# Optimization experiments

Measured on AMD Instinct MI355X. Metric: run time of the kernel, lower is better.

The kernel has to match this reference:

```python
import jax, jax.numpy as jnp
import numpy as np

N = 4096      # nodes
IN = 512      # in_dim
HID = 64      # hid_dim
OUT = 8       # out_dim (classes)
H = 2         # num_heads / meta-paths
SEM = 32      # semantic attention hidden size
P_EDGE = 0.005  # edge probability -> avg degree ~20


def setup_inputs() -> dict:
    key = jax.random.key(0)
    ks = jax.random.split(key, 12)
    h = jax.random.normal(ks[0], (N, IN), jnp.float32)
    # sparse binary adjacency per head, with self-loops (densified as in adj.to_dense())
    adj = (jax.random.uniform(ks[1], (H, N, N)) < P_EDGE).astype(jnp.float32)
    adj = jnp.clip(adj + jnp.eye(N, dtype=jnp.float32)[None], 0.0, 1.0)
    sc = lambda k, s: (jax.random.normal(k, s, jnp.float32) * 0.05)
    W1 = sc(ks[2], (H, IN, HID))
    b1 = jnp.zeros((H, HID), jnp.float32)
    Wq = sc(ks[3], (H, HID, HID)); bq = jnp.zeros((H, HID), jnp.float32)
    Wk = sc(ks[4], (H, HID, HID)); bk = jnp.zeros((H, HID), jnp.float32)
    Wv = sc(ks[5], (H, HID, HID)); bv = jnp.zeros((H, HID), jnp.float32)
    sem_W1 = sc(ks[6], (HID, SEM)); sem_b1 = jnp.zeros((SEM,), jnp.float32)
    sem_W2 = sc(ks[7], (SEM, 1))
    pred_W = sc(ks[8], (HID, OUT)); pred_b = jnp.zeros((OUT,), jnp.float32)
    return dict(h=h, adj=adj, W1=W1, b1=b1, Wq=Wq, bq=bq, Wk=Wk, bk=bk,
                Wv=Wv, bv=bv, sem_W1=sem_W1, sem_b1=sem_b1, sem_W2=sem_W2,
                pred_W=pred_W, pred_b=pred_b)


def reference(h, adj, W1, b1, Wq, bq, Wk, bk, Wv, bv,
              sem_W1, sem_b1, sem_W2, pred_W, pred_b):
    def embed(adj_i, W1_i, b1_i, Wq_i, bq_i, Wk_i, bk_i, Wv_i, bv_i):
        # GraphConvolution (Kipf): adj @ (h @ W) + b, then ReLU
        x = jax.nn.relu(adj_i @ (h @ W1_i) + b1_i)            # [N, HID]
        Q = x @ Wq_i + bq_i
        K = x @ Wk_i + bk_i
        V = x @ Wv_i + bv_i
        # dense-masked attention: adj.to_dense() * (Q K^T), softmax over rows
        A_tilde = adj_i * (Q @ K.T)                            # [N, N]
        att = jax.nn.softmax(A_tilde, axis=1)
        # gcn_norm: symmetric D^{-1/2} A D^{-1/2}, degree = row sums
        d = att.sum(axis=1)
        dinv = jnp.where(d > 0, jax.lax.rsqrt(d), 0.0)
        att_n = dinv[:, None] * att * dinv[None, :]
        return jax.nn.relu(att_n @ V)                          # [N, HID]

    z = jax.vmap(embed)(adj, W1, b1, Wq, bq, Wk, bk, Wv, bv)   # [H, N, HID]
    z = jnp.transpose(z, (1, 0, 2))                            # [N, H, HID]
    # SemanticAttention: project -> mean over nodes -> softmax over dim=1
    w = jnp.tanh(z @ sem_W1 + sem_b1) @ sem_W2                 # [N, H, 1]
    w = w.mean(axis=0)                                         # [H, 1]
    beta = jax.nn.softmax(w, axis=1)  # faithful to torch.softmax(w, dim=1)
    p2 = (beta[None] * z).sum(axis=1)                          # [N, HID]
    return jax.nn.softmax(p2 @ pred_W + pred_b, axis=1)        # [N, OUT]
```

## Files before the change

kernel.cpp:

```cpp
#include <hip/hip_runtime.h>
#include <hip/hip_bf16.h>

#define NN   4096
#define IND  512
#define HIDD 64
#define OUTD 8
#define NH   2
#define CAP  128

using bf16 = __hip_bfloat16;

__device__ __forceinline__ float b2f(bf16 v) { return __bfloat162float(v); }

__device__ __forceinline__ bool sniff_bf(const unsigned* __restrict__ adjw) {
    return (adjw[0] & 0xFFFFu) == 0x3F80u;
}
__device__ __forceinline__ float ldf(const void* p, int i, bool isbf) {
    return isbf ? b2f(((const bf16*)p)[i]) : ((const float*)p)[i];
}
__device__ __forceinline__ void load8f(const void* p, size_t off, bool isbf, float* o) {
    if (isbf) {
        uint4 d = *reinterpret_cast<const uint4*>((const bf16*)p + off);
        unsigned u[4] = {d.x, d.y, d.z, d.w};
#pragma unroll
        for (int w = 0; w < 4; ++w) {
            o[2 * w]     = __uint_as_float(u[w] << 16);
            o[2 * w + 1] = __uint_as_float(u[w] & 0xFFFF0000u);
        }
    } else {
        const float* q = (const float*)p + off;
        float4 a = *reinterpret_cast<const float4*>(q);
        float4 b = *reinterpret_cast<const float4*>(q + 4);
        o[0] = a.x; o[1] = a.y; o[2] = a.z; o[3] = a.w;
        o[4] = b.x; o[5] = b.y; o[6] = b.z; o[7] = b.w;
    }
}
__device__ __forceinline__ void load8_f32(const float* q, float* o) {
    float4 a = *reinterpret_cast<const float4*>(q);
    float4 b = *reinterpret_cast<const float4*>(q + 4);
    o[0] = a.x; o[1] = a.y; o[2] = a.z; o[3] = a.w;
    o[4] = b.x; o[5] = b.y; o[6] = b.z; o[7] = b.w;
}

__global__ void __launch_bounds__(256) k1_csr_hw(const void* __restrict__ h,
                                                 const void* __restrict__ W1,
                                                 const void* __restrict__ adjv,
                                                 int* __restrict__ deg,
                                                 int* __restrict__ cols,
                                                 float* __restrict__ hW,
                                                 float* __restrict__ vsum) {
    __shared__ __align__(16) float As[64][36];
    __shared__ __align__(16) float Bs[64][68];
    __shared__ int s_cnt;
    __shared__ int s_lc[CAP];
    const bool isbf = sniff_bf((const unsigned*)adjv);
    const int bx = blockIdx.x;
    const int tid = threadIdx.x;
    if (bx == 0 && tid < NH * HIDD) vsum[tid] = 0.f;

    if (bx < 256) {
        int head = bx >> 7;
        int i0 = (bx & 127) * 32;
        size_t wOff = (size_t)head * IND * HIDD;
        int r0 = (tid >> 4) * 2;
        int c0 = (tid & 15) * 4;
        float acc[2][4] = {};
        for (int kc = 0; kc < IND; kc += 64) {
            {
                int row = tid >> 3;
                int kp  = (tid & 7) * 8;
                float t8[8];
                load8f(h, (size_t)(i0 + row) * IND + kc + kp, isbf, t8);
#pragma unroll
                for (int j = 0; j < 8; ++j) As[kp + j][row] = t8[j];
            }
            {
                int kb = tid >> 2;
                int cp = (tid & 3) * 16;
                float t8[8];
                load8f(W1, wOff + (size_t)(kc + kb) * HIDD + cp, isbf, t8);
#pragma unroll
                for (int j = 0; j < 8; ++j) Bs[kb][cp + j] = t8[j];
                load8f(W1, wOff + (size_t)(kc + kb) * HIDD + cp + 8, isbf, t8);
#pragma unroll
                for (int j = 0; j < 8; ++j) Bs[kb][cp + 8 + j] = t8[j];
            }
            __syncthreads();
#pragma unroll 8
            for (int k = 0; k < 64; ++k) {
                float2 a2 = *reinterpret_cast<const float2*>(&As[k][r0]);
                float4 b4 = *reinterpret_cast<const float4*>(&Bs[k][c0]);
                float bb[4] = {b4.x, b4.y, b4.z, b4.w};
#pragma unroll
                for (int ib = 0; ib < 4; ++ib) {
                    acc[0][ib] = fmaf(a2.x, bb[ib], acc[0][ib]);
                    acc[1][ib] = fmaf(a2.y, bb[ib], acc[1][ib]);
                }
            }
            __syncthreads();
        }
        float* Ch = hW + (size_t)head * NN * HIDD;
#pragma unroll
        for (int ia = 0; ia < 2; ++ia)
            *reinterpret_cast<float4*>(Ch + (size_t)(i0 + r0 + ia) * HIDD + c0) =
                make_float4(acc[ia][0], acc[ia][1], acc[ia][2], acc[ia][3]);
        return;
    }
    int row = bx - 256;
    if (tid == 0) s_cnt = 0;
    __syncthreads();
    if (isbf) {
        const uint4* a4 = reinterpret_cast<const uint4*>((const bf16*)adjv + (size_t)row * NN);
#pragma unroll
        for (int it = 0; it < 2; ++it) {
            int v = tid + it * 256;
            uint4 d = a4[v];
            unsigned u[4] = {d.x, d.y, d.z, d.w};
            int base = v * 8;
#pragma unroll
            for (int w = 0; w < 4; ++w) {
                if (u[w] & 0xFFFFu) { int p = atomicAdd(&s_cnt, 1); if (p < CAP) s_lc[p] = base + 2 * w; }
                if (u[w] >> 16)     { int p = atomicAdd(&s_cnt, 1); if (p < CAP) s_lc[p] = base + 2 * w + 1; }
            }
        }
    } else {
        const uint4* a4 = reinterpret_cast<const uint4*>((const float*)adjv + (size_t)row * NN);
#pragma unroll
        for (int it = 0; it < 4; ++it) {
            int v = tid + it * 256;
            uint4 d = a4[v];
            unsigned u[4] = {d.x, d.y, d.z, d.w};
            int base = v * 4;
#pragma unroll
            for (int w = 0; w < 4; ++w) {
                if (u[w]) { int p = atomicAdd(&s_cnt, 1); if (p < CAP) s_lc[p] = base + w; }
            }
        }
    }
    __syncthreads();
    int c = s_cnt; if (c > CAP) c = CAP;
    if (tid == 0) deg[row] = c;
    int* oc = cols + (size_t)row * CAP;
    for (int k = tid; k < c; k += 256) oc[k] = s_lc[k];
}

__global__ void k_aggx(const float* __restrict__ hW, const void* __restrict__ b1,
                       const void* __restrict__ adjv,
                       const int* __restrict__ deg, const int* __restrict__ cols,
                       float* __restrict__ x) {
    bool isbf = sniff_bf((const unsigned*)adjv);
    int h = blockIdx.y;
    int i = blockIdx.x * 4 + threadIdx.y;
    int t = threadIdx.x;
    const float* hWh = hW + (size_t)h * NN * HIDD;
    int r = h * NN + i;
    int d = deg[r];
    const int* cl = cols + (size_t)r * CAP;
    float acc = ldf(b1, h * HIDD + t, isbf);
    int e = 0;
    for (; e + 4 <= d; e += 4) {
        int c0 = cl[e], c1 = cl[e + 1], c2 = cl[e + 2], c3 = cl[e + 3];
        float v0 = hWh[(size_t)c0 * HIDD + t];
        float v1 = hWh[(size_t)c1 * HIDD + t];
        float v2 = hWh[(size_t)c2 * HIDD + t];
        float v3 = hWh[(size_t)c3 * HIDD + t];
        acc += (v0 + v1) + (v2 + v3);
    }
    for (; e < d; ++e) acc += hWh[(size_t)cl[e] * HIDD + t];
    x[(size_t)r * HIDD + t] = fmaxf(acc, 0.f);
}

__global__ void __launch_bounds__(256) k_qkv(const float* __restrict__ x,
                                             const void* Wq, const void* bq,
                                             const void* Wk, const void* bk,
                                             const void* Wv, const void* bv,
                                             const void* __restrict__ adjv,
                                             float* Q, float* K, float* V,
                                             float* __restrict__ vsum) {
    __shared__ __align__(16) float xs[64][36];
    __shared__ __align__(16) float Ws[64][68];
    __shared__ float vred[HIDD];
    bool isbf = sniff_bf((const unsigned*)adjv);
    int tid = threadIdx.x;
    int z = blockIdx.x >> 8;
    int rem = blockIdx.x & 255;
    int head = rem >> 7;
    int i0 = (rem & 127) * 32;
    const void* W  = (z == 0) ? Wq : (z == 1) ? Wk : Wv;
    const void* bb = (z == 0) ? bq : (z == 1) ? bk : bv;
    float* C = ((z == 0) ? Q : (z == 1) ? K : V) + (size_t)head * NN * HIDD;
    const float* xh = x + (size_t)head * NN * HIDD;
    {
        int row = tid >> 3;
        int kp  = (tid & 7) * 8;
        float t8[8];
        load8_f32(xh + (size_t)(i0 + row) * HIDD + kp, t8);
#pragma unroll
        for (int j = 0; j < 8; ++j) xs[kp + j][row] = t8[j];
    }
    {
        int kb = tid >> 2;
        int cp = (tid & 3) * 16;
        size_t base = (size_t)head * HIDD * HIDD + (size_t)kb * HIDD + cp;
        float t8[8];
        load8f(W, base, isbf, t8);
#pragma unroll
        for (int j = 0; j < 8; ++j) Ws[kb][cp + j] = t8[j];
        load8f(W, base + 8, isbf, t8);
#pragma unroll
        for (int j = 0; j < 8; ++j) Ws[kb][cp + 8 + j] = t8[j];
    }
    if (tid < HIDD) vred[tid] = 0.f;
    __syncthreads();
    int r0 = (tid >> 4) * 2;
    int c0 = (tid & 15) * 4;
    float acc[2][4] = {};
#pragma unroll 8
    for (int k = 0; k < HIDD; ++k) {
        float2 a2 = *reinterpret_cast<const float2*>(&xs[k][r0]);
        float4 b4 = *reinterpret_cast<const float4*>(&Ws[k][c0]);
        float bbv[4] = {b4.x, b4.y, b4.z, b4.w};
#pragma unroll
        for (int ib = 0; ib < 4; ++ib) {
            acc[0][ib] = fmaf(a2.x, bbv[ib], acc[0][ib]);
            acc[1][ib] = fmaf(a2.y, bbv[ib], acc[1][ib]);
        }
    }
    float bz[4];
#pragma unroll
    for (int ib = 0; ib < 4; ++ib) bz[ib] = ldf(bb, head * HIDD + c0 + ib, isbf);
#pragma unroll
    for (int ia = 0; ia < 2; ++ia)
        *reinterpret_cast<float4*>(C + (size_t)(i0 + r0 + ia) * HIDD + c0) =
            make_float4(acc[ia][0] + bz[0], acc[ia][1] + bz[1],
                        acc[ia][2] + bz[2], acc[ia][3] + bz[3]);
    if (z == 2) {
#pragma unroll
        for (int ib = 0; ib < 4; ++ib)
            atomicAdd(&vred[c0 + ib], acc[0][ib] + acc[1][ib] + 2.f * bz[ib]);
        __syncthreads();
        if (tid < HIDD) atomicAdd(&vsum[head * HIDD + tid], vred[tid]);
    }
}

__global__ void __launch_bounds__(256) k_attn(const float* __restrict__ Q,
                                              const float* __restrict__ Km,
                                              const float* __restrict__ V,
                                              const float* __restrict__ vsum,
                                              const int* __restrict__ deg,
                                              const int* __restrict__ cols,
                                              const void* __restrict__ predW,
                                              const void* __restrict__ predb,
                                              const void* __restrict__ adjv,
                                              void* __restrict__ outv) {
    bool isbf = sniff_bf((const unsigned*)adjv);
    int wid = threadIdx.x >> 6;
    int t   = threadIdx.x & 63;
    int i   = blockIdx.x * 4 + wid;
    __shared__ __align__(16) float qs[4][64];
    __shared__ float wgt[4][CAP];
    __shared__ int   cs[4][CAP];
    __shared__ float p2s[4][64];
    float p2 = 0.f;

    for (int h = 0; h < NH; ++h) {
        int r = h * NN + i;
        int d = deg[r];
        const int* cl   = cols + (size_t)r * CAP;
        const float* Qh = Q + (size_t)h * NN * HIDD;
        const float* Kh = Km + (size_t)h * NN * HIDD;
        const float* Vh = V + (size_t)h * NN * HIDD;
        qs[wid][t] = Qh[(size_t)i * HIDD + t];
        for (int e = t; e < d; e += 64) cs[wid][e] = cl[e];

        float s0 = 0.f, s1 = 0.f;
        float lmax = 0.f;
        const float4* q4 = reinterpret_cast<const float4*>(qs[wid]);
        if (t < d) {
            const float4* K4 = reinterpret_cast<const float4*>(Kh + (size_t)cs[wid][t] * HIDD);
            float s = 0.f;
#pragma unroll 4
            for (int k = 0; k < 16; ++k) {
                float4 kv = K4[k]; float4 qv = q4[k];
                s += qv.x * kv.x + qv.y * kv.y + qv.z * kv.z + qv.w * kv.w;
            }
            s0 = s; lmax = fmaxf(lmax, s);
        }
        if (t + 64 < d) {
            const float4* K4 = reinterpret_cast<const float4*>(Kh + (size_t)cs[wid][t + 64] * HIDD);
            float s = 0.f;
#pragma unroll 4
            for (int k = 0; k < 16; ++k) {
                float4 kv = K4[k]; float4 qv = q4[k];
                s += qv.x * kv.x + qv.y * kv.y + qv.z * kv.z + qv.w * kv.w;
            }
            s1 = s; lmax = fmaxf(lmax, s);
        }
#pragma unroll
        for (int off = 32; off; off >>= 1) lmax = fmaxf(lmax, __shfl_xor(lmax, off));
        float m  = lmax;
        float eb = __expf(-m);
        float lsum = 0.f;
        if (t < d)      { float w = __expf(s0 - m); lsum += w; wgt[wid][t] = w - eb; }
        if (t + 64 < d) { float w = __expf(s1 - m); lsum += w; wgt[wid][t + 64] = w - eb; }
#pragma unroll
        for (int off = 32; off; off >>= 1) lsum += __shfl_xor(lsum, off);
        float Z = lsum + (float)(NN - d) * eb;
        float c = 1.f / Z;

        float acc = eb * vsum[h * HIDD + t];
        int e = 0;
        for (; e + 4 <= d; e += 4) {
            float w0 = wgt[wid][e], w1 = wgt[wid][e + 1];
            float w2 = wgt[wid][e + 2], w3 = wgt[wid][e + 3];
            int c0 = cs[wid][e], c1 = cs[wid][e + 1];
            int c2 = cs[wid][e + 2], c3 = cs[wid][e + 3];
            float v0 = Vh[(size_t)c0 * HIDD + t];
            float v1 = Vh[(size_t)c1 * HIDD + t];
            float v2 = Vh[(size_t)c2 * HIDD + t];
            float v3 = Vh[(size_t)c3 * HIDD + t];
            acc += w0 * v0 + w1 * v1 + w2 * v2 + w3 * v3;
        }
        for (; e < d; ++e) acc += wgt[wid][e] * Vh[(size_t)cs[wid][e] * HIDD + t];
        p2 += fmaxf(acc * c, 0.f);
    }

    p2s[wid][t] = p2;
    if (t < OUTD) {
        float a = ldf(predb, t, isbf);
#pragma unroll 8
        for (int k = 0; k < HIDD; ++k) a += p2s[wid][k] * ldf(predW, k * OUTD + t, isbf);
        float mx = a;
#pragma unroll
        for (int off = 4; off; off >>= 1) mx = fmaxf(mx, __shfl_xor(mx, off));
        float e = __expf(a - mx);
        float s = e;
#pragma unroll
        for (int off = 4; off; off >>= 1) s += __shfl_xor(s, off);
        float v = e / s;
        if (isbf) ((bf16*)outv)[(size_t)i * OUTD + t] = __float2bfloat16(v);
        else      ((float*)outv)[(size_t)i * OUTD + t] = v;
    }
}

extern "C" void kernel_launch(void* const* d_in, const int* in_sizes, int n_in,
                              void* d_out, int out_size, void* d_ws, size_t ws_size,
                              hipStream_t stream) {
    const void* adj = d_in[1];

    char* w = (char*)d_ws;
    int*   deg  = (int*)w;                        w += (size_t)NH * NN * 4;
    int*   cols = (int*)w;                        w += (size_t)NH * NN * CAP * 4;
    float* hW   = (float*)w;                      w += (size_t)NH * NN * HIDD * 4;
    float* x    = (float*)w;                      w += (size_t)NH * NN * HIDD * 4;
    float* Q    = (float*)w;                      w += (size_t)NH * NN * HIDD * 4;
    float* K    = (float*)w;                      w += (size_t)NH * NN * HIDD * 4;
    float* V    = (float*)w;                      w += (size_t)NH * NN * HIDD * 4;
    float* vsum = (float*)w;                      w += (size_t)NH * HIDD * 4;

    k1_csr_hw<<<256 + NH * NN, 256, 0, stream>>>(d_in[0], d_in[2], adj, deg, cols, hW, vsum);
    k_aggx   <<<dim3(NN / 4, NH), dim3(64, 4), 0, stream>>>(hW, d_in[3], adj, deg, cols, x);
    k_qkv    <<<768, 256, 0, stream>>>(x, d_in[4], d_in[5], d_in[6], d_in[7],
                                       d_in[8], d_in[9], adj, Q, K, V, vsum);
    k_attn   <<<NN / 4, 256, 0, stream>>>(Q, K, V, vsum, deg, cols, d_in[13], d_in[14],
                                          adj, d_out);
}
```

Measured before the change: 256.2 us.

## Fuse aggregation, QKV and attention kernels into one persistent kernel with grid barriers

Merges the three post-CSR kernels (neighbour aggregation, QKV projection, sparse attention with prediction) into a single 1024-block kernel that separates the phases with software grid barriers built on global atomics. Shared memory for the phases is overlaid through a union. The aim is to remove two kernel launch gaps and their tail effects. The cost is spin-wait barriers that assume all 1024 blocks are co-resident (launch_bounds 256,4), plus a bounded spin timeout that could break correctness if residency is not met.

```diff
diff --git a/kernel.cpp b/kernel.cpp
--- a/kernel.cpp
+++ b/kernel.cpp
@@ -7,6 +7,7 @@
 #define OUTD 8
 #define NH   2
 #define CAP  128
+#define FBLK 1024
 
 using bf16 = __hip_bfloat16;
 
@@ -48,7 +49,8 @@
                                                  int* __restrict__ deg,
                                                  int* __restrict__ cols,
                                                  float* __restrict__ hW,
-                                                 float* __restrict__ vsum) {
+                                                 float* __restrict__ vsum,
+                                                 int* __restrict__ bar) {
     __shared__ __align__(16) float As[64][36];
     __shared__ __align__(16) float Bs[64][68];
     __shared__ int s_cnt;
@@ -56,7 +58,10 @@
     const bool isbf = sniff_bf((const unsigned*)adjv);
     const int bx = blockIdx.x;
     const int tid = threadIdx.x;
-    if (bx == 0 && tid < NH * HIDD) vsum[tid] = 0.f;
+    if (bx == 0) {
+        if (tid < NH * HIDD) vsum[tid] = 0.f;
+        if (tid < 8) bar[tid] = 0;
+    }
 
     if (bx < 256) {
         int head = bx >> 7;
@@ -144,202 +149,210 @@
     for (int k = tid; k < c; k += 256) oc[k] = s_lc[k];
 }
 
-__global__ void k_aggx(const float* __restrict__ hW, const void* __restrict__ b1,
-                       const void* __restrict__ adjv,
-                       const int* __restrict__ deg, const int* __restrict__ cols,
-                       float* __restrict__ x) {
-    bool isbf = sniff_bf((const unsigned*)adjv);
-    int h = blockIdx.y;
-    int i = blockIdx.x * 4 + threadIdx.y;
-    int t = threadIdx.x;
-    const float* hWh = hW + (size_t)h * NN * HIDD;
-    int r = h * NN + i;
-    int d = deg[r];
-    const int* cl = cols + (size_t)r * CAP;
-    float acc = ldf(b1, h * HIDD + t, isbf);
-    int e = 0;
-    for (; e + 4 <= d; e += 4) {
-        int c0 = cl[e], c1 = cl[e + 1], c2 = cl[e + 2], c3 = cl[e + 3];
-        float v0 = hWh[(size_t)c0 * HIDD + t];
-        float v1 = hWh[(size_t)c1 * HIDD + t];
-        float v2 = hWh[(size_t)c2 * HIDD + t];
-        float v3 = hWh[(size_t)c3 * HIDD + t];
-        acc += (v0 + v1) + (v2 + v3);
-    }
-    for (; e < d; ++e) acc += hWh[(size_t)cl[e] * HIDD + t];
-    x[(size_t)r * HIDD + t] = fmaxf(acc, 0.f);
-}
-
-__global__ void __launch_bounds__(256) k_qkv(const float* __restrict__ x,
-                                             const void* Wq, const void* bq,
-                                             const void* Wk, const void* bk,
-                                             const void* Wv, const void* bv,
-                                             const void* __restrict__ adjv,
-                                             float* Q, float* K, float* V,
-                                             float* __restrict__ vsum) {
-    __shared__ __align__(16) float xs[64][36];
-    __shared__ __align__(16) float Ws[64][68];
-    __shared__ float vred[HIDD];
-    bool isbf = sniff_bf((const unsigned*)adjv);
-    int tid = threadIdx.x;
-    int z = blockIdx.x >> 8;
-    int rem = blockIdx.x & 255;
-    int head = rem >> 7;
-    int i0 = (rem & 127) * 32;
-    const void* W  = (z == 0) ? Wq : (z == 1) ? Wk : Wv;
-    const void* bb = (z == 0) ? bq : (z == 1) ? bk : bv;
-    float* C = ((z == 0) ? Q : (z == 1) ? K : V) + (size_t)head * NN * HIDD;
-    const float* xh = x + (size_t)head * NN * HIDD;
+__device__ __forceinline__ void gridbar(int* bar, int tid) {
+    __builtin_amdgcn_s_waitcnt(0);
+    __syncthreads();
+    if (tid == 0) {
+        __threadfence();
+        __hip_atomic_fetch_add(bar, 1, __ATOMIC_RELEASE, __HIP_MEMORY_SCOPE_AGENT);
+        long spins = 0;
+        while (__hip_atomic_load(bar, __ATOMIC_RELAXED, __HIP_MEMORY_SCOPE_AGENT) < FBLK
+               && ++spins < 4000000L)
+            __builtin_amdgcn_s_sleep(2);
+        __threadfence();
+    }
+    __syncthreads();
+}
+
+struct FArgs {
+    const void *b1, *Wq, *bq, *Wk, *bk, *Wv, *bv, *pW, *pb, *adj;
+    const int *deg, *cols;
+    const float *hW;
+    float *x, *Q, *K, *V, *vsum;
+    int *bar;
+    void *out;
+};
+
+__global__ void __launch_bounds__(256, 4) k_fused(FArgs a) {
+    __shared__ __align__(16) union {
+        struct { float xs[64][36]; float Ws[64][68]; float vred[64]; } q;
+        struct { float qs[4][64]; float wgt[4][CAP]; int cs[4][CAP]; float p2s[4][64]; } t;
+    } su;
+    const bool isbf = sniff_bf((const unsigned*)a.adj);
+    const int bx = blockIdx.x;
+    const int tid = threadIdx.x;
+    const int wv = tid >> 6;
+    const int t  = tid & 63;
+
     {
-        int row = tid >> 3;
-        int kp  = (tid & 7) * 8;
-        float t8[8];
-        load8_f32(xh + (size_t)(i0 + row) * HIDD + kp, t8);
-#pragma unroll
-        for (int j = 0; j < 8; ++j) xs[kp + j][row] = t8[j];
-    }
+        int g = bx * 4 + wv;
+#pragma unroll
+        for (int rr = 0; rr < 2; ++rr) {
+            int r = g * 2 + rr;
+            int h = r >> 12;
+            const float* hWh = a.hW + (size_t)h * NN * HIDD;
+            int d = a.deg[r];
+            const int* cl = a.cols + (size_t)r * CAP;
+            float acc = ldf(a.b1, h * HIDD + t, isbf);
+            int e = 0;
+            for (; e + 4 <= d; e += 4) {
+                int c0 = cl[e], c1 = cl[e + 1], c2 = cl[e + 2], c3 = cl[e + 3];
+                float v0 = hWh[(size_t)c0 * HIDD + t];
+                float v1 = hWh[(size_t)c1 * HIDD + t];
+                float v2 = hWh[(size_t)c2 * HIDD + t];
+                float v3 = hWh[(size_t)c3 * HIDD + t];
+                acc += (v0 + v1) + (v2 + v3);
+            }
+            for (; e < d; ++e) acc += hWh[(size_t)cl[e] * HIDD + t];
+            a.x[(size_t)r * HIDD + t] = fmaxf(acc, 0.f);
+        }
+    }
+    gridbar(&a.bar[0], tid);
+
+    if (bx < 768) {
+        int z = bx >> 8;
+        int rem = bx & 255;
+        int head = rem >> 7;
+        int i0 = (rem & 127) * 32;
+        const void* W  = (z == 0) ? a.Wq : (z == 1) ? a.Wk : a.Wv;
+        const void* bb = (z == 0) ? a.bq : (z == 1) ? a.bk : a.bv;
+        float* C = ((z == 0) ? a.Q : (z == 1) ? a.K : a.V) + (size_t)head * NN * HIDD;
+        const float* xh = a.x + (size_t)head * NN * HIDD;
+        {
+            int row = tid >> 3;
+            int kp  = (tid & 7) * 8;
+            float t8[8];
+            load8_f32(xh + (size_t)(i0 + row) * HIDD + kp, t8);
+#pragma unroll
+            for (int j = 0; j < 8; ++j) su.q.xs[kp + j][row] = t8[j];
+        }
+        {
+            int kb = tid >> 2;
+            int cp = (tid & 3) * 16;
+            size_t base = (size_t)head * HIDD * HIDD + (size_t)kb * HIDD + cp;
+            float t8[8];
+            load8f(W, base, isbf, t8);
+#pragma unroll
+            for (int j = 0; j < 8; ++j) su.q.Ws[kb][cp + j] = t8[j];
+            load8f(W, base + 8, isbf, t8);
+#pragma unroll
+            for (int j = 0; j < 8; ++j) su.q.Ws[kb][cp + 8 + j] = t8[j];
+        }
+        if (tid < HIDD) su.q.vred[tid] = 0.f;
+        __syncthreads();
+        int r0 = (tid >> 4) * 2;
+        int c0 = (tid & 15) * 4;
+        float acc[2][4] = {};
+#pragma unroll 8
+        for (int k = 0; k < HIDD; ++k) {
+            float2 a2 = *reinterpret_cast<const float2*>(&su.q.xs[k][r0]);
+            float4 b4 = *reinterpret_cast<const float4*>(&su.q.Ws[k][c0]);
+            float bbv[4] = {b4.x, b4.y, b4.z, b4.w};
+#pragma unroll
+            for (int ib = 0; ib < 4; ++ib) {
+                acc[0][ib] = fmaf(a2.x, bbv[ib], acc[0][ib]);
+                acc[1][ib] = fmaf(a2.y, bbv[ib], acc[1][ib]);
+            }
+        }
+        float bz[4];
+#pragma unroll
+        for (int ib = 0; ib < 4; ++ib) bz[ib] = ldf(bb, head * HIDD + c0 + ib, isbf);
+#pragma unroll
+        for (int ia = 0; ia < 2; ++ia)
+            *reinterpret_cast<float4*>(C + (size_t)(i0 + r0 + ia) * HIDD + c0) =
+                make_float4(acc[ia][0] + bz[0], acc[ia][1] + bz[1],
+                            acc[ia][2] + bz[2], acc[ia][3] + bz[3]);
+        if (z == 2) {
+#pragma unroll
+            for (int ib = 0; ib < 4; ++ib)
+                atomicAdd(&su.q.vred[c0 + ib], acc[0][ib] + acc[1][ib] + 2.f * bz[ib]);
+            __syncthreads();
+            if (tid < HIDD) atomicAdd(&a.vsum[head * HIDD + tid], su.q.vred[tid]);
+        }
+    }
+    gridbar(&a.bar[1], tid);
+
     {
-        int kb = tid >> 2;
-        int cp = (tid & 3) * 16;
-        size_t base = (size_t)head * HIDD * HIDD + (size_t)kb * HIDD + cp;
-        float t8[8];
-        load8f(W, base, isbf, t8);
-#pragma unroll
-        for (int j = 0; j < 8; ++j) Ws[kb][cp + j] = t8[j];
-        load8f(W, base + 8, isbf, t8);
-#pragma unroll
-        for (int j = 0; j < 8; ++j) Ws[kb][cp + 8 + j] = t8[j];
-    }
-    if (tid < HIDD) vred[tid] = 0.f;
-    __syncthreads();
-    int r0 = (tid >> 4) * 2;
-    int c0 = (tid & 15) * 4;
-    float acc[2][4] = {};
+        int i = bx * 4 + wv;
+        float p2 = 0.f;
+        for (int h = 0; h < NH; ++h) {
+            int r = h * NN + i;
+            int d = a.deg[r];
+            const int* cl   = a.cols + (size_t)r * CAP;
+            const float* Qh = a.Q + (size_t)h * NN * HIDD;
+            const float* Kh = a.K + (size_t)h * NN * HIDD;
+            const float* Vh = a.V + (size_t)h * NN * HIDD;
+            su.t.qs[wv][t] = Qh[(size_t)i * HIDD + t];
+            for (int e = t; e < d; e += 64) su.t.cs[wv][e] = cl[e];
+
+            float s0 = 0.f, s1 = 0.f;
+            float lmax = 0.f;
+            const float4* q4 = reinterpret_cast<const float4*>(su.t.qs[wv]);
+            if (t < d) {
+                const float4* K4 = reinterpret_cast<const float4*>(Kh + (size_t)su.t.cs[wv][t] * HIDD);
+                float s = 0.f;
+#pragma unroll 4
+                for (int k = 0; k < 16; ++k) {
+                    float4 kv = K4[k]; float4 qv = q4[k];
+                    s += qv.x * kv.x + qv.y * kv.y + qv.z * kv.z + qv.w * kv.w;
+                }
+                s0 = s; lmax = fmaxf(lmax, s);
+            }
+            if (t + 64 < d) {
+                const float4* K4 = reinterpret_cast<const float4*>(Kh + (size_t)su.t.cs[wv][t + 64] * HIDD);
+                float s = 0.f;
+#pragma unroll 4
+                for (int k = 0; k < 16; ++k) {
+                    float4 kv = K4[k]; float4 qv = q4[k];
+                    s += qv.x * kv.x + qv.y * kv.y + qv.z * kv.z + qv.w * kv.w;
+                }
+                s1 = s; lmax = fmaxf(lmax, s);
+            }
+#pragma unroll
+            for (int off = 32; off; off >>= 1) lmax = fmaxf(lmax, __shfl_xor(lmax, off));
+            float m  = lmax;
+            float eb = __expf(-m);
+            float lsum = 0.f;
+            if (t < d)      { float w = __expf(s0 - m); lsum += w; su.t.wgt[wv][t] = w - eb; }
+            if (t + 64 < d) { float w = __expf(s1 - m); lsum += w; su.t.wgt[wv][t + 64] = w - eb; }
+#pragma unroll
+            for (int off = 32; off; off >>= 1) lsum += __shfl_xor(lsum, off);
+            float Z = lsum + (float)(NN - d) * eb;
+            float c = 1.f / Z;
+
+            float acc = eb * a.vsum[h * HIDD + t];
+            int e = 0;
+            for (; e + 4 <= d; e += 4) {
+                float w0 = su.t.wgt[wv][e],     w1 = su.t.wgt[wv][e + 1];
+                float w2 = su.t.wgt[wv][e + 2], w3 = su.t.wgt[wv][e + 3];
+                int c0 = su.t.cs[wv][e],     c1 = su.t.cs[wv][e + 1];
+                int c2 = su.t.cs[wv][e + 2], c3 = su.t.cs[wv][e + 3];
+                float v0 = Vh[(size_t)c0 * HIDD + t];
+                float v1 = Vh[(size_t)c1 * HIDD + t];
+                float v2 = Vh[(size_t)c2 * HIDD + t];
+                float v3 = Vh[(size_t)c3 * HIDD + t];
+                acc += w0 * v0 + w1 * v1 + w2 * v2 + w3 * v3;
+            }
+            for (; e < d; ++e) acc += su.t.wgt[wv][e] * Vh[(size_t)su.t.cs[wv][e] * HIDD + t];
+            p2 += fmaxf(acc * c, 0.f);
+        }
+
+        su.t.p2s[wv][t] = p2;
+        if (t < OUTD) {
+            float o = ldf(a.pb, t, isbf);
 #pragma unroll 8
-    for (int k = 0; k < HIDD; ++k) {
-        float2 a2 = *reinterpret_cast<const float2*>(&xs[k][r0]);
-        float4 b4 = *reinterpret_cast<const float4*>(&Ws[k][c0]);
-        float bbv[4] = {b4.x, b4.y, b4.z, b4.w};
-#pragma unroll
-        for (int ib = 0; ib < 4; ++ib) {
-            acc[0][ib] = fmaf(a2.x, bbv[ib], acc[0][ib]);
-            acc[1][ib] = fmaf(a2.y, bbv[ib], acc[1][ib]);
-        }
-    }
-    float bz[4];
-#pragma unroll
-    for (int ib = 0; ib < 4; ++ib) bz[ib] = ldf(bb, head * HIDD + c0 + ib, isbf);
-#pragma unroll
-    for (int ia = 0; ia < 2; ++ia)
-        *reinterpret_cast<float4*>(C + (size_t)(i0 + r0 + ia) * HIDD + c0) =
-            make_float4(acc[ia][0] + bz[0], acc[ia][1] + bz[1],
-                        acc[ia][2] + bz[2], acc[ia][3] + bz[3]);
-    if (z == 2) {
-#pragma unroll
-        for (int ib = 0; ib < 4; ++ib)
-            atomicAdd(&vred[c0 + ib], acc[0][ib] + acc[1][ib] + 2.f * bz[ib]);
-        __syncthreads();
-        if (tid < HIDD) atomicAdd(&vsum[head * HIDD + tid], vred[tid]);
-    }
-}
-
-__global__ void __launch_bounds__(256) k_attn(const float* __restrict__ Q,
-                                              const float* __restrict__ Km,
-                                              const float* __restrict__ V,
-                                              const float* __restrict__ vsum,
-                                              const int* __restrict__ deg,
-                                              const int* __restrict__ cols,
-                                              const void* __restrict__ predW,
-                                              const void* __restrict__ predb,
-                                              const void* __restrict__ adjv,
-                                              void* __restrict__ outv) {
-    bool isbf = sniff_bf((const unsigned*)adjv);
-    int wid = threadIdx.x >> 6;
-    int t   = threadIdx.x & 63;
-    int i   = blockIdx.x * 4 + wid;
-    __shared__ __align__(16) float qs[4][64];
-    __shared__ float wgt[4][CAP];
-    __shared__ int   cs[4][CAP];
-    __shared__ float p2s[4][64];
-    float p2 = 0.f;
-
-    for (int h = 0; h < NH; ++h) {
-        int r = h * NN + i;
-        int d = deg[r];
-        const int* cl   = cols + (size_t)r * CAP;
-        const float* Qh = Q + (size_t)h * NN * HIDD;
-        const float* Kh = Km + (size_t)h * NN * HIDD;
-        const float* Vh = V + (size_t)h * NN * HIDD;
-        qs[wid][t] = Qh[(size_t)i * HIDD + t];
-        for (int e = t; e < d; e += 64) cs[wid][e] = cl[e];
-
-        float s0 = 0.f, s1 = 0.f;
-        float lmax = 0.f;
-        const float4* q4 = reinterpret_cast<const float4*>(qs[wid]);
-        if (t < d) {
-            const float4* K4 = reinterpret_cast<const float4*>(Kh + (size_t)cs[wid][t] * HIDD);
-            float s = 0.f;
-#pragma unroll 4
-            for (int k = 0; k < 16; ++k) {
-                float4 kv = K4[k]; float4 qv = q4[k];
-                s += qv.x * kv.x + qv.y * kv.y + qv.z * kv.z + qv.w * kv.w;
-            }
-            s0 = s; lmax = fmaxf(lmax, s);
-        }
-        if (t + 64 < d) {
-            const float4* K4 = reinterpret_cast<const float4*>(Kh + (size_t)cs[wid][t + 64] * HIDD);
-            float s = 0.f;
-#pragma unroll 4
-            for (int k = 0; k < 16; ++k) {
-                float4 kv = K4[k]; float4 qv = q4[k];
-                s += qv.x * kv.x + qv.y * kv.y + qv.z * kv.z + qv.w * kv.w;
-            }
-            s1 = s; lmax = fmaxf(lmax, s);
-        }
-#pragma unroll
-        for (int off = 32; off; off >>= 1) lmax = fmaxf(lmax, __shfl_xor(lmax, off));
-        float m  = lmax;
-        float eb = __expf(-m);
-        float lsum = 0.f;
-        if (t < d)      { float w = __expf(s0 - m); lsum += w; wgt[wid][t] = w - eb; }
-        if (t + 64 < d) { float w = __expf(s1 - m); lsum += w; wgt[wid][t + 64] = w - eb; }
-#pragma unroll
-        for (int off = 32; off; off >>= 1) lsum += __shfl_xor(lsum, off);
-        float Z = lsum + (float)(NN - d) * eb;
-        float c = 1.f / Z;
-
-        float acc = eb * vsum[h * HIDD + t];
-        int e = 0;
-        for (; e + 4 <= d; e += 4) {
-            float w0 = wgt[wid][e], w1 = wgt[wid][e + 1];
-            float w2 = wgt[wid][e + 2], w3 = wgt[wid][e + 3];
-            int c0 = cs[wid][e], c1 = cs[wid][e + 1];
-            int c2 = cs[wid][e + 2], c3 = cs[wid][e + 3];
-            float v0 = Vh[(size_t)c0 * HIDD + t];
-            float v1 = Vh[(size_t)c1 * HIDD + t];
-            float v2 = Vh[(size_t)c2 * HIDD + t];
-            float v3 = Vh[(size_t)c3 * HIDD + t];
-            acc += w0 * v0 + w1 * v1 + w2 * v2 + w3 * v3;
-        }
-        for (; e < d; ++e) acc += wgt[wid][e] * Vh[(size_t)cs[wid][e] * HIDD + t];
-        p2 += fmaxf(acc * c, 0.f);
-    }
-
-    p2s[wid][t] = p2;
-    if (t < OUTD) {
-        float a = ldf(predb, t, isbf);
-#pragma unroll 8
-        for (int k = 0; k < HIDD; ++k) a += p2s[wid][k] * ldf(predW, k * OUTD + t, isbf);
-        float mx = a;
-#pragma unroll
-        for (int off = 4; off; off >>= 1) mx = fmaxf(mx, __shfl_xor(mx, off));
-        float e = __expf(a - mx);
-        float s = e;
-#pragma unroll
-        for (int off = 4; off; off >>= 1) s += __shfl_xor(s, off);
-        float v = e / s;
-        if (isbf) ((bf16*)outv)[(size_t)i * OUTD + t] = __float2bfloat16(v);
-        else      ((float*)outv)[(size_t)i * OUTD + t] = v;
+            for (int k = 0; k < HIDD; ++k) o += su.t.p2s[wv][k] * ldf(a.pW, k * OUTD + t, isbf);
+            float mx = o;
+#pragma unroll
+            for (int off = 4; off; off >>= 1) mx = fmaxf(mx, __shfl_xor(mx, off));
+            float e = __expf(o - mx);
+            float s = e;
+#pragma unroll
+            for (int off = 4; off; off >>= 1) s += __shfl_xor(s, off);
+            float v = e / s;
+            if (isbf) ((bf16*)a.out)[(size_t)i * OUTD + t] = __float2bfloat16(v);
+            else      ((float*)a.out)[(size_t)i * OUTD + t] = v;
+        }
     }
 }
 
@@ -357,11 +370,14 @@
     float* K    = (float*)w;                      w += (size_t)NH * NN * HIDD * 4;
     float* V    = (float*)w;                      w += (size_t)NH * NN * HIDD * 4;
     float* vsum = (float*)w;                      w += (size_t)NH * HIDD * 4;
-
-    k1_csr_hw<<<256 + NH * NN, 256, 0, stream>>>(d_in[0], d_in[2], adj, deg, cols, hW, vsum);
-    k_aggx   <<<dim3(NN / 4, NH), dim3(64, 4), 0, stream>>>(hW, d_in[3], adj, deg, cols, x);
-    k_qkv    <<<768, 256, 0, stream>>>(x, d_in[4], d_in[5], d_in[6], d_in[7],
-                                       d_in[8], d_in[9], adj, Q, K, V, vsum);
-    k_attn   <<<NN / 4, 256, 0, stream>>>(Q, K, V, vsum, deg, cols, d_in[13], d_in[14],
-                                          adj, d_out);
-}
+    int*   bar  = (int*)w;                        w += 256;
+
+    k1_csr_hw<<<256 + NH * NN, 256, 0, stream>>>(d_in[0], d_in[2], adj, deg, cols,
+                                                 hW, vsum, bar);
+    FArgs fa;
+    fa.b1 = d_in[3]; fa.Wq = d_in[4]; fa.bq = d_in[5]; fa.Wk = d_in[6]; fa.bk = d_in[7];
+    fa.Wv = d_in[8]; fa.bv = d_in[9]; fa.pW = d_in[13]; fa.pb = d_in[14]; fa.adj = adj;
+    fa.deg = deg; fa.cols = cols; fa.hW = hW; fa.x = x;
+    fa.Q = Q; fa.K = K; fa.V = V; fa.vsum = vsum; fa.bar = bar; fa.out = d_out;
+    k_fused<<<FBLK, 256, 0, stream>>>(fa);
+}
```

After: 483.3 us. 1.89x slower.
